# Kernel tuning notes

Measured on AMD Instinct MI355X. Metric: run time of the kernel, lower is better.

The kernel has to match this reference:

```python
import jax, jax.numpy as jnp
import numpy as np

N_NODES = 100000
D_FEAT = 128
N_EDGES = 1600000


def setup_inputs() -> dict:
    key = jax.random.key(0)
    k1, k2, k3 = jax.random.split(key, 3)
    x = jax.random.normal(k1, (N_NODES, D_FEAT), dtype=jnp.float32)
    edge_weight = jax.random.uniform(k2, (N_EDGES,), dtype=jnp.float32)
    edge_index = jax.random.randint(k3, (2, N_EDGES), 0, N_NODES, dtype=jnp.int64)
    return {"x": x, "edge_weight": edge_weight, "edge_index": edge_index, "n_nodes": N_NODES}


def reference(x, edge_weight, edge_index, n_nodes):
    # h_v = sum_{(u->v) in E} w_uv * h_u  (gather -> scale -> scatter_add)
    src = edge_index[0]
    dst = edge_index[1]
    msg = x[src] * edge_weight[:, None]          # (E, d)
    out = jax.ops.segment_sum(msg, dst, num_segments=n_nodes)  # (N, d)
    return out
```

## Files before the change

### kernel.cpp

```cpp
#include <hip/hip_runtime.h>
#include <hip/hip_bf16.h>


constexpr int D_FEAT = 128;
constexpr int NPB = 128;
constexpr int SBLK = 256;
constexpr int LOG_SBLK = 8;
constexpr int STILE = 2048;
constexpr int CAP = 3072;

typedef float v4f __attribute__((ext_vector_type(4)));

__global__ __launch_bounds__(256) void scatter_atomic_kernel(
    const float* __restrict__ x, const float* __restrict__ w,
    const int* __restrict__ src_idx, const int* __restrict__ dst_idx,
    float* __restrict__ out, int n_edges) {
  long long tid = (long long)blockIdx.x * blockDim.x + threadIdx.x;
  int lane = (int)(tid & 31);
  long long e = tid >> 5;
  if (e >= n_edges) return;
  int s = src_idx[e];
  int d = dst_idx[e];
  float wt = w[e];
  float4 v = ((const float4*)(x + (size_t)s * D_FEAT))[lane];
  float* o = out + (size_t)d * D_FEAT + (size_t)lane * 4;
  atomicAdd(o + 0, v.x * wt);
  atomicAdd(o + 1, v.y * wt);
  atomicAdd(o + 2, v.z * wt);
  atomicAdd(o + 3, v.w * wt);
}

__device__ __forceinline__ int block_excl_scan(int v, int* sh, int* total) {
  const int lane = threadIdx.x & 63;
  const int wid = threadIdx.x >> 6;
  const int nw = blockDim.x >> 6;
  int inc = v;
  #pragma unroll
  for (int o = 1; o < 64; o <<= 1) {
    int t = __shfl_up(inc, o, 64);
    if (lane >= o) inc += t;
  }
  if (lane == 63) sh[wid] = inc;
  __syncthreads();
  if (threadIdx.x == 0) {
    int a = 0;
    for (int k = 0; k < nw; ++k) { int t = sh[k]; sh[k] = a; a += t; }
    sh[nw] = a;
  }
  __syncthreads();
  int r = sh[wid] + inc - v;
  if (total) *total = sh[nw];
  __syncthreads();
  return r;
}

__global__ __launch_bounds__(512) void hist_kernel(
    const int* __restrict__ dst, int* __restrict__ hist, int n_edges,
    int nbk, int tile) {
  __shared__ int h[1024];
  const int tid = threadIdx.x;
  const int b = blockIdx.x;
  for (int i = tid; i < nbk; i += 512) h[i] = 0;
  __syncthreads();
  int base = b * tile;
  int lim = min(base + tile, n_edges);
  for (int i = base + tid; i < lim; i += 512)
    atomicAdd(&h[((unsigned)dst[i]) >> 7], 1);
  __syncthreads();
  for (int k = tid; k < nbk; k += 512) hist[b * nbk + k] = h[k];
}

__global__ __launch_bounds__(256) void scan_kernel(
    const int* __restrict__ hist, int* __restrict__ off_flat,
    unsigned long long* __restrict__ tstate, int nbk, int n_edges) {
  __shared__ int sh[9];
  __shared__ int s_prefix;
  const int tid = threadIdx.x;
  const int blk = blockIdx.x;
  const int n_scan = nbk * SBLK;
  const int base = blk * STILE + tid * 8;

  int c[8];
  #pragma unroll
  for (int k = 0; k < 8; ++k) {
    int i = base + k;
    c[k] = (i < n_scan) ? hist[(i & (SBLK - 1)) * nbk + (i >> LOG_SBLK)] : 0;
  }
  int p[8];
  int tsum = 0;
  #pragma unroll
  for (int k = 0; k < 8; ++k) { p[k] = tsum; tsum += c[k]; }

  int total;
  int tex = block_excl_scan(tsum, sh, &total);

  if (tid == 0) {
    int excl = 0;
    if (blk == 0) {
      __hip_atomic_store(&tstate[0], (2ULL << 32) | (unsigned)total,
                         __ATOMIC_RELEASE, __HIP_MEMORY_SCOPE_AGENT);
    } else {
      __hip_atomic_store(&tstate[blk], (1ULL << 32) | (unsigned)total,
                         __ATOMIC_RELEASE, __HIP_MEMORY_SCOPE_AGENT);
      int pidx = blk - 1;
      int run = 0;
      while (true) {
        unsigned long long v = __hip_atomic_load(
            &tstate[pidx], __ATOMIC_ACQUIRE, __HIP_MEMORY_SCOPE_AGENT);
        unsigned st = (unsigned)(v >> 32);
        if (st != 1u && st != 2u) { __builtin_amdgcn_s_sleep(1); continue; }
        run += (int)(unsigned)v;
        if (st == 2u) break;
        --pidx;
      }
      excl = run;
      __hip_atomic_store(&tstate[blk],
                         (2ULL << 32) | (unsigned)(excl + total),
                         __ATOMIC_RELEASE, __HIP_MEMORY_SCOPE_AGENT);
    }
    s_prefix = excl;
  }
  __syncthreads();

  int my = s_prefix + tex;
  if (base + 8 <= n_scan) {
    ((int4*)(off_flat + base))[0] =
        make_int4(my + p[0], my + p[1], my + p[2], my + p[3]);
    ((int4*)(off_flat + base))[1] =
        make_int4(my + p[4], my + p[5], my + p[6], my + p[7]);
  } else {
    #pragma unroll
    for (int k = 0; k < 8; ++k)
      if (base + k < n_scan) off_flat[base + k] = my + p[k];
  }
  if (blk == 0 && tid == 0) off_flat[n_scan] = n_edges;
}

__global__ __launch_bounds__(512) void scatter_kernel(
    const int* __restrict__ src, const int* __restrict__ dst,
    const float* __restrict__ w, const int* __restrict__ off_flat,
    uint2* __restrict__ csr, int n_edges, int nbk, int tile) {
  __shared__ int cur[1024];
  const int tid = threadIdx.x;
  const int b = blockIdx.x;
  for (int k = tid; k < nbk; k += 512) cur[k] = off_flat[k * SBLK + b];
  __syncthreads();
  int base = b * tile;
  int lim = min(base + tile, n_edges);
  for (int i = base + tid; i < lim; i += 512) {
    unsigned d = (unsigned)dst[i];
    unsigned k = d >> 7;
    unsigned dl = d & 127u;
    int pos = atomicAdd(&cur[k], 1);
    csr[pos] = make_uint2((unsigned)src[i] | (dl << 20), __float_as_uint(w[i]));
  }
}

__global__ __launch_bounds__(512) void gather_kernel(
    const float* __restrict__ x, const int* __restrict__ off_flat,
    const uint2* __restrict__ csr, float* __restrict__ out, int n_nodes) {
  __shared__ uint2 eds[CAP];
  __shared__ unsigned short perm[CAP];
  __shared__ int loff[NPB + 1];
  __shared__ int lcur[NPB];
  __shared__ int sh[9];

  const int b = blockIdx.x;
  const int tid = threadIdx.x;
  const int beg = off_flat[b * SBLK];
  const int end = off_flat[(b + 1) * SBLK];
  const int cnt = end - beg;
  const int nbase = b * NPB;

  const int wv = tid >> 6;
  const int lane = tid & 63;
  const int f = lane & 31;
  const int half = lane >> 5;
  const float4* X = (const float4*)x;

  if (cnt <= CAP) {
    if (tid < NPB) lcur[tid] = 0;
    __syncthreads();
    for (int i = tid; i < cnt; i += 512) {
      uint2 e = csr[beg + i];
      eds[i] = e;
      atomicAdd(&lcur[e.x >> 20], 1);
    }
    __syncthreads();
    {
      int v = (tid < NPB) ? lcur[tid] : 0;
      int ex = block_excl_scan(v, sh, nullptr);
      __syncthreads();
      if (tid < NPB) { loff[tid] = ex; lcur[tid] = 0; }
      if (tid == 0) loff[NPB] = cnt;
    }
    __syncthreads();
    for (int i = tid; i < cnt; i += 512) {
      int dl = eds[i].x >> 20;
      int pos = loff[dl] + atomicAdd(&lcur[dl], 1);
      perm[pos] = (unsigned short)i;
    }
    __syncthreads();

    for (int n = wv; n < NPB; n += 8) {
      int node = nbase + n;
      if (node >= n_nodes) break;
      int jb = loff[n];
      int je = loff[n + 1];
      float4 a0 = make_float4(0.f, 0.f, 0.f, 0.f);
      float4 a1 = make_float4(0.f, 0.f, 0.f, 0.f);
      float4 a2 = make_float4(0.f, 0.f, 0.f, 0.f);
      float4 a3 = make_float4(0.f, 0.f, 0.f, 0.f);
      int j = jb + half;
      for (; j + 6 < je; j += 8) {
        uint2 e0 = eds[perm[j]];
        uint2 e1 = eds[perm[j + 2]];
        uint2 e2 = eds[perm[j + 4]];
        uint2 e3 = eds[perm[j + 6]];
        float4 v0 = X[(size_t)(e0.x & 0xFFFFFu) * 32 + f];
        float4 v1 = X[(size_t)(e1.x & 0xFFFFFu) * 32 + f];
        float4 v2 = X[(size_t)(e2.x & 0xFFFFFu) * 32 + f];
        float4 v3 = X[(size_t)(e3.x & 0xFFFFFu) * 32 + f];
        float w0 = __uint_as_float(e0.y);
        float w1 = __uint_as_float(e1.y);
        float w2 = __uint_as_float(e2.y);
        float w3 = __uint_as_float(e3.y);
        a0.x += w0 * v0.x; a0.y += w0 * v0.y; a0.z += w0 * v0.z; a0.w += w0 * v0.w;
        a1.x += w1 * v1.x; a1.y += w1 * v1.y; a1.z += w1 * v1.z; a1.w += w1 * v1.w;
        a2.x += w2 * v2.x; a2.y += w2 * v2.y; a2.z += w2 * v2.z; a2.w += w2 * v2.w;
        a3.x += w3 * v3.x; a3.y += w3 * v3.y; a3.z += w3 * v3.z; a3.w += w3 * v3.w;
      }
      for (; j < je; j += 2) {
        uint2 e0 = eds[perm[j]];
        float4 v0 = X[(size_t)(e0.x & 0xFFFFFu) * 32 + f];
        float w0 = __uint_as_float(e0.y);
        a0.x += w0 * v0.x; a0.y += w0 * v0.y; a0.z += w0 * v0.z; a0.w += w0 * v0.w;
      }
      a0.x += a1.x + a2.x + a3.x;
      a0.y += a1.y + a2.y + a3.y;
      a0.z += a1.z + a2.z + a3.z;
      a0.w += a1.w + a2.w + a3.w;
      a0.x += __shfl_xor(a0.x, 32, 64);
      a0.y += __shfl_xor(a0.y, 32, 64);
      a0.z += __shfl_xor(a0.z, 32, 64);
      a0.w += __shfl_xor(a0.w, 32, 64);
      if (half == 0) {
        v4f val = {a0.x, a0.y, a0.z, a0.w};
        __builtin_nontemporal_store(val, (v4f*)out + (size_t)node * 32 + f);
      }
    }
  } else {
    for (int n = wv; n < NPB; n += 8) {
      int node = nbase + n;
      if (node >= n_nodes) break;
      float4 a0 = make_float4(0.f, 0.f, 0.f, 0.f);
      for (int j = half; j < cnt; j += 2) {
        uint2 e = csr[beg + j];
        if ((int)(e.x >> 20) == n) {
          float4 v = X[(size_t)(e.x & 0xFFFFFu) * 32 + f];
          float wt = __uint_as_float(e.y);
          a0.x += wt * v.x; a0.y += wt * v.y; a0.z += wt * v.z; a0.w += wt * v.w;
        }
      }
      a0.x += __shfl_xor(a0.x, 32, 64);
      a0.y += __shfl_xor(a0.y, 32, 64);
      a0.z += __shfl_xor(a0.z, 32, 64);
      a0.w += __shfl_xor(a0.w, 32, 64);
      if (half == 0) {
        v4f val = {a0.x, a0.y, a0.z, a0.w};
        __builtin_nontemporal_store(val, (v4f*)out + (size_t)node * 32 + f);
      }
    }
  }
}

extern "C" void kernel_launch(void* const* d_in, const int* in_sizes, int n_in,
                              void* d_out, int out_size, void* d_ws, size_t ws_size,
                              hipStream_t stream) {
  const float* x  = (const float*)d_in[0];
  const float* w  = (const float*)d_in[1];
  const int* eidx = (const int*)d_in[2];

  int n_edges = in_sizes[1];
  int n_nodes = out_size / D_FEAT;
  const int* src = eidx;
  const int* dst = eidx + n_edges;
  float* out = (float*)d_out;

  const int nbk = (n_nodes + NPB - 1) / NPB;
  const int tile = (n_edges + SBLK - 1) / SBLK;
  const int n_scan = nbk * SBLK;
  const int ntiles = (n_scan + STILE - 1) / STILE;

  const size_t n_hist = (size_t)SBLK * nbk;
  const size_t n_off = (size_t)n_scan + 4;
  size_t need = (n_hist + n_off) * 4 + 128 * 8 + (size_t)n_edges * 8;
  if (ws_size < need || nbk > 1024 || ntiles > 128 || n_nodes >= (1 << 20)) {
    hipMemsetAsync(d_out, 0, (size_t)out_size * sizeof(float), stream);
    long long total_threads = (long long)n_edges * 32;
    long long grid = (total_threads + 255) / 256;
    scatter_atomic_kernel<<<(dim3)(unsigned)grid, 256, 0, stream>>>(
        x, w, src, dst, out, n_edges);
    return;
  }

  int* hist = (int*)d_ws;
  int* off_flat = hist + n_hist;
  unsigned long long* tstate = (unsigned long long*)(off_flat + n_off);
  uint2* csr = (uint2*)(tstate + 128);

  hist_kernel<<<SBLK, 512, 0, stream>>>(dst, hist, n_edges, nbk, tile);
  scan_kernel<<<ntiles, 256, 0, stream>>>(hist, off_flat, tstate, nbk,
                                          n_edges);
  scatter_kernel<<<SBLK, 512, 0, stream>>>(src, dst, w, off_flat, csr,
                                           n_edges, nbk, tile);
  gather_kernel<<<nbk, 512, 0, stream>>>(x, off_flat, csr, out, n_nodes);
}
```

Before: 269.0 us.

## Split gather blocks by feature half and parallelize scan lookback across a wavefront

```diff
diff --git a/kernel.cpp b/kernel.cpp
--- a/kernel.cpp
+++ b/kernel.cpp
@@ -94,31 +94,49 @@
   int total;
   int tex = block_excl_scan(tsum, sh, &total);
 
-  if (tid == 0) {
-    int excl = 0;
-    if (blk == 0) {
+  if (blk == 0) {
+    if (tid == 0) {
       __hip_atomic_store(&tstate[0], (2ULL << 32) | (unsigned)total,
                          __ATOMIC_RELEASE, __HIP_MEMORY_SCOPE_AGENT);
-    } else {
+      s_prefix = 0;
+    }
+  } else {
+    if (tid == 0)
       __hip_atomic_store(&tstate[blk], (1ULL << 32) | (unsigned)total,
                          __ATOMIC_RELEASE, __HIP_MEMORY_SCOPE_AGENT);
-      int pidx = blk - 1;
+    if (tid < 64) {
+      int pidx = blk - 1 - tid;
       int run = 0;
       while (true) {
-        unsigned long long v = __hip_atomic_load(
-            &tstate[pidx], __ATOMIC_ACQUIRE, __HIP_MEMORY_SCOPE_AGENT);
-        unsigned st = (unsigned)(v >> 32);
-        if (st != 1u && st != 2u) { __builtin_amdgcn_s_sleep(1); continue; }
-        run += (int)(unsigned)v;
-        if (st == 2u) break;
-        --pidx;
-      }
-      excl = run;
-      __hip_atomic_store(&tstate[blk],
-                         (2ULL << 32) | (unsigned)(excl + total),
-                         __ATOMIC_RELEASE, __HIP_MEMORY_SCOPE_AGENT);
-    }
-    s_prefix = excl;
+        unsigned long long v;
+        unsigned st;
+        if (pidx >= 0) {
+          do {
+            v = __hip_atomic_load(&tstate[pidx], __ATOMIC_ACQUIRE,
+                                  __HIP_MEMORY_SCOPE_AGENT);
+            st = (unsigned)(v >> 32);
+            if (st != 1u && st != 2u) __builtin_amdgcn_s_sleep(1);
+          } while (st != 1u && st != 2u);
+        } else {
+          v = (2ULL << 32);
+          st = 2u;
+        }
+        unsigned long long pmask = __ballot(st == 2u);
+        int lfirst = (int)__ffsll((long long)pmask) - 1;
+        int contrib = (lfirst < 0 || tid <= lfirst) ? (int)(unsigned)v : 0;
+        #pragma unroll
+        for (int o = 32; o; o >>= 1) contrib += __shfl_xor(contrib, o, 64);
+        run += contrib;
+        if (lfirst >= 0) break;
+        pidx -= 64;
+      }
+      if (tid == 0) {
+        __hip_atomic_store(&tstate[blk],
+                           (2ULL << 32) | (unsigned)(run + total),
+                           __ATOMIC_RELEASE, __HIP_MEMORY_SCOPE_AGENT);
+        s_prefix = run;
+      }
+    }
   }
   __syncthreads();
 
@@ -156,7 +174,7 @@
   }
 }
 
-__global__ __launch_bounds__(512) void gather_kernel(
+__global__ __launch_bounds__(256) void gather_kernel(
     const float* __restrict__ x, const int* __restrict__ off_flat,
     const uint2* __restrict__ csr, float* __restrict__ out, int n_nodes) {
   __shared__ uint2 eds[CAP];
@@ -165,7 +183,8 @@
   __shared__ int lcur[NPB];
   __shared__ int sh[9];
 
-  const int b = blockIdx.x;
+  const int b = blockIdx.x >> 1;
+  const int fh = blockIdx.x & 1;
   const int tid = threadIdx.x;
   const int beg = off_flat[b * SBLK];
   const int end = off_flat[(b + 1) * SBLK];
@@ -174,14 +193,14 @@
 
   const int wv = tid >> 6;
   const int lane = tid & 63;
-  const int f = lane & 31;
-  const int half = lane >> 5;
+  const int q = lane >> 4;
+  const int f = (lane & 15) + fh * 16;
   const float4* X = (const float4*)x;
 
   if (cnt <= CAP) {
     if (tid < NPB) lcur[tid] = 0;
     __syncthreads();
-    for (int i = tid; i < cnt; i += 512) {
+    for (int i = tid; i < cnt; i += 256) {
       uint2 e = csr[beg + i];
       eds[i] = e;
       atomicAdd(&lcur[e.x >> 20], 1);
@@ -195,14 +214,14 @@
       if (tid == 0) loff[NPB] = cnt;
     }
     __syncthreads();
-    for (int i = tid; i < cnt; i += 512) {
+    for (int i = tid; i < cnt; i += 256) {
       int dl = eds[i].x >> 20;
       int pos = loff[dl] + atomicAdd(&lcur[dl], 1);
       perm[pos] = (unsigned short)i;
     }
     __syncthreads();
 
-    for (int n = wv; n < NPB; n += 8) {
+    for (int n = wv; n < NPB; n += 4) {
       int node = nbase + n;
       if (node >= n_nodes) break;
       int jb = loff[n];
@@ -211,12 +230,12 @@
       float4 a1 = make_float4(0.f, 0.f, 0.f, 0.f);
       float4 a2 = make_float4(0.f, 0.f, 0.f, 0.f);
       float4 a3 = make_float4(0.f, 0.f, 0.f, 0.f);
-      int j = jb + half;
-      for (; j + 6 < je; j += 8) {
+      int j = jb + q;
+      for (; j + 12 < je; j += 16) {
         uint2 e0 = eds[perm[j]];
-        uint2 e1 = eds[perm[j + 2]];
-        uint2 e2 = eds[perm[j + 4]];
-        uint2 e3 = eds[perm[j + 6]];
+        uint2 e1 = eds[perm[j + 4]];
+        uint2 e2 = eds[perm[j + 8]];
+        uint2 e3 = eds[perm[j + 12]];
         float4 v0 = X[(size_t)(e0.x & 0xFFFFFu) * 32 + f];
         float4 v1 = X[(size_t)(e1.x & 0xFFFFFu) * 32 + f];
         float4 v2 = X[(size_t)(e2.x & 0xFFFFFu) * 32 + f];
@@ -230,7 +249,7 @@
         a2.x += w2 * v2.x; a2.y += w2 * v2.y; a2.z += w2 * v2.z; a2.w += w2 * v2.w;
         a3.x += w3 * v3.x; a3.y += w3 * v3.y; a3.z += w3 * v3.z; a3.w += w3 * v3.w;
       }
-      for (; j < je; j += 2) {
+      for (; j < je; j += 4) {
         uint2 e0 = eds[perm[j]];
         float4 v0 = X[(size_t)(e0.x & 0xFFFFFu) * 32 + f];
         float w0 = __uint_as_float(e0.y);
@@ -240,21 +259,25 @@
       a0.y += a1.y + a2.y + a3.y;
       a0.z += a1.z + a2.z + a3.z;
       a0.w += a1.w + a2.w + a3.w;
+      a0.x += __shfl_xor(a0.x, 16, 64);
+      a0.y += __shfl_xor(a0.y, 16, 64);
+      a0.z += __shfl_xor(a0.z, 16, 64);
+      a0.w += __shfl_xor(a0.w, 16, 64);
       a0.x += __shfl_xor(a0.x, 32, 64);
       a0.y += __shfl_xor(a0.y, 32, 64);
       a0.z += __shfl_xor(a0.z, 32, 64);
       a0.w += __shfl_xor(a0.w, 32, 64);
-      if (half == 0) {
+      if (q == 0) {
         v4f val = {a0.x, a0.y, a0.z, a0.w};
         __builtin_nontemporal_store(val, (v4f*)out + (size_t)node * 32 + f);
       }
     }
   } else {
-    for (int n = wv; n < NPB; n += 8) {
+    for (int n = wv; n < NPB; n += 4) {
       int node = nbase + n;
       if (node >= n_nodes) break;
       float4 a0 = make_float4(0.f, 0.f, 0.f, 0.f);
-      for (int j = half; j < cnt; j += 2) {
+      for (int j = q; j < cnt; j += 4) {
         uint2 e = csr[beg + j];
         if ((int)(e.x >> 20) == n) {
           float4 v = X[(size_t)(e.x & 0xFFFFFu) * 32 + f];
@@ -262,11 +285,15 @@
           a0.x += wt * v.x; a0.y += wt * v.y; a0.z += wt * v.z; a0.w += wt * v.w;
         }
       }
+      a0.x += __shfl_xor(a0.x, 16, 64);
+      a0.y += __shfl_xor(a0.y, 16, 64);
+      a0.z += __shfl_xor(a0.z, 16, 64);
+      a0.w += __shfl_xor(a0.w, 16, 64);
       a0.x += __shfl_xor(a0.x, 32, 64);
       a0.y += __shfl_xor(a0.y, 32, 64);
       a0.z += __shfl_xor(a0.z, 32, 64);
       a0.w += __shfl_xor(a0.w, 32, 64);
-      if (half == 0) {
+      if (q == 0) {
         v4f val = {a0.x, a0.y, a0.z, a0.w};
         __builtin_nontemporal_store(val, (v4f*)out + (size_t)node * 32 + f);
       }
@@ -314,5 +341,5 @@
                                           n_edges);
   scatter_kernel<<<SBLK, 512, 0, stream>>>(src, dst, w, off_flat, csr,
                                            n_edges, nbk, tile);
-  gather_kernel<<<nbk, 512, 0, stream>>>(x, off_flat, csr, out, n_nodes);
-}
+  gather_kernel<<<nbk * 2, 256, 0, stream>>>(x, off_flat, csr, out, n_nodes);
+}
```

Result: no change. 267.4 us (-0.6%).

## Replace per-block histogram scan with global bucket counts and LDS-staged coalesced scatter

Applied to the files above, without the earlier changes.

```diff
diff --git a/kernel.cpp b/kernel.cpp
--- a/kernel.cpp
+++ b/kernel.cpp
@@ -1,12 +1,11 @@
 #include <hip/hip_runtime.h>
-#include <hip/hip_bf16.h>
 
 
 constexpr int D_FEAT = 128;
 constexpr int NPB = 128;
-constexpr int SBLK = 256;
-constexpr int LOG_SBLK = 8;
-constexpr int STILE = 2048;
+constexpr int NBK_MAX = 1024;
+constexpr int HBLK = 256;
+constexpr int CTILE = 3136;
 constexpr int CAP = 3072;
 
 typedef float v4f __attribute__((ext_vector_type(4)));
@@ -55,109 +54,109 @@
 }
 
 __global__ __launch_bounds__(512) void hist_kernel(
-    const int* __restrict__ dst, int* __restrict__ hist, int n_edges,
-    int nbk, int tile) {
-  __shared__ int h[1024];
+    const int* __restrict__ dst, int* __restrict__ gtot,
+    int* __restrict__ gcur, int* __restrict__ gbase, int* __restrict__ done,
+    int n_edges, int nbk, int tile) {
+  __shared__ int h[NBK_MAX];
+  __shared__ int sh[9];
+  __shared__ int slast;
   const int tid = threadIdx.x;
   const int b = blockIdx.x;
-  for (int i = tid; i < nbk; i += 512) h[i] = 0;
+  for (int k = tid; k < nbk; k += 512) h[k] = 0;
   __syncthreads();
   int base = b * tile;
   int lim = min(base + tile, n_edges);
   for (int i = base + tid; i < lim; i += 512)
     atomicAdd(&h[((unsigned)dst[i]) >> 7], 1);
   __syncthreads();
-  for (int k = tid; k < nbk; k += 512) hist[b * nbk + k] = h[k];
-}
-
-__global__ __launch_bounds__(256) void scan_kernel(
-    const int* __restrict__ hist, int* __restrict__ off_flat,
-    unsigned long long* __restrict__ tstate, int nbk, int n_edges) {
-  __shared__ int sh[9];
-  __shared__ int s_prefix;
-  const int tid = threadIdx.x;
-  const int blk = blockIdx.x;
-  const int n_scan = nbk * SBLK;
-  const int base = blk * STILE + tid * 8;
-
-  int c[8];
-  #pragma unroll
-  for (int k = 0; k < 8; ++k) {
-    int i = base + k;
-    c[k] = (i < n_scan) ? hist[(i & (SBLK - 1)) * nbk + (i >> LOG_SBLK)] : 0;
-  }
-  int p[8];
-  int tsum = 0;
-  #pragma unroll
-  for (int k = 0; k < 8; ++k) { p[k] = tsum; tsum += c[k]; }
-
-  int total;
-  int tex = block_excl_scan(tsum, sh, &total);
-
-  if (tid == 0) {
-    int excl = 0;
-    if (blk == 0) {
-      __hip_atomic_store(&tstate[0], (2ULL << 32) | (unsigned)total,
-                         __ATOMIC_RELEASE, __HIP_MEMORY_SCOPE_AGENT);
-    } else {
-      __hip_atomic_store(&tstate[blk], (1ULL << 32) | (unsigned)total,
-                         __ATOMIC_RELEASE, __HIP_MEMORY_SCOPE_AGENT);
-      int pidx = blk - 1;
-      int run = 0;
-      while (true) {
-        unsigned long long v = __hip_atomic_load(
-            &tstate[pidx], __ATOMIC_ACQUIRE, __HIP_MEMORY_SCOPE_AGENT);
-        unsigned st = (unsigned)(v >> 32);
-        if (st != 1u && st != 2u) { __builtin_amdgcn_s_sleep(1); continue; }
-        run += (int)(unsigned)v;
-        if (st == 2u) break;
-        --pidx;
-      }
-      excl = run;
-      __hip_atomic_store(&tstate[blk],
-                         (2ULL << 32) | (unsigned)(excl + total),
-                         __ATOMIC_RELEASE, __HIP_MEMORY_SCOPE_AGENT);
-    }
-    s_prefix = excl;
-  }
-  __syncthreads();
-
-  int my = s_prefix + tex;
-  if (base + 8 <= n_scan) {
-    ((int4*)(off_flat + base))[0] =
-        make_int4(my + p[0], my + p[1], my + p[2], my + p[3]);
-    ((int4*)(off_flat + base))[1] =
-        make_int4(my + p[4], my + p[5], my + p[6], my + p[7]);
-  } else {
-    #pragma unroll
-    for (int k = 0; k < 8; ++k)
-      if (base + k < n_scan) off_flat[base + k] = my + p[k];
-  }
-  if (blk == 0 && tid == 0) off_flat[n_scan] = n_edges;
+  for (int k = tid; k < nbk; k += 512)
+    if (h[k]) atomicAdd(&gtot[k], h[k]);
+  __threadfence();
+  __syncthreads();
+  if (tid == 0)
+    slast = (__hip_atomic_fetch_add(done, 1, __ATOMIC_ACQ_REL,
+                                    __HIP_MEMORY_SCOPE_AGENT) ==
+             (int)gridDim.x - 1);
+  __syncthreads();
+  if (slast) {
+    int carry = 0;
+    for (int kb = 0; kb < nbk; kb += 512) {
+      int k = kb + tid;
+      int v = (k < nbk)
+                  ? __hip_atomic_load(&gtot[k], __ATOMIC_RELAXED,
+                                      __HIP_MEMORY_SCOPE_AGENT)
+                  : 0;
+      int tot;
+      int ex = block_excl_scan(v, sh, &tot);
+      if (k < nbk) { gbase[k] = carry + ex; gcur[k] = carry + ex; }
+      carry += tot;
+    }
+    if (tid == 0) gbase[nbk] = carry;
+  }
 }
 
 __global__ __launch_bounds__(512) void scatter_kernel(
     const int* __restrict__ src, const int* __restrict__ dst,
-    const float* __restrict__ w, const int* __restrict__ off_flat,
+    const float* __restrict__ w, int* __restrict__ gcur,
     uint2* __restrict__ csr, int n_edges, int nbk, int tile) {
-  __shared__ int cur[1024];
+  __shared__ uint2 ed[CTILE];
+  __shared__ unsigned short bkt[CTILE];
+  __shared__ unsigned int prm[CTILE];
+  __shared__ int h[NBK_MAX];
+  __shared__ int lb[NBK_MAX];
+  __shared__ int cur[NBK_MAX];
+  __shared__ int gb[NBK_MAX];
+  __shared__ int sh[9];
+
   const int tid = threadIdx.x;
   const int b = blockIdx.x;
-  for (int k = tid; k < nbk; k += 512) cur[k] = off_flat[k * SBLK + b];
-  __syncthreads();
   int base = b * tile;
   int lim = min(base + tile, n_edges);
+  int cnt = max(lim - base, 0);
+
+  for (int k = tid; k < nbk; k += 512) { h[k] = 0; cur[k] = 0; }
+  __syncthreads();
   for (int i = base + tid; i < lim; i += 512) {
+    int j = i - base;
     unsigned d = (unsigned)dst[i];
     unsigned k = d >> 7;
-    unsigned dl = d & 127u;
-    int pos = atomicAdd(&cur[k], 1);
-    csr[pos] = make_uint2((unsigned)src[i] | (dl << 20), __float_as_uint(w[i]));
-  }
-}
-
-__global__ __launch_bounds__(512) void gather_kernel(
-    const float* __restrict__ x, const int* __restrict__ off_flat,
+    ed[j] = make_uint2((unsigned)src[i] | ((d & 127u) << 20),
+                       __float_as_uint(w[i]));
+    bkt[j] = (unsigned short)k;
+    atomicAdd(&h[k], 1);
+  }
+  __syncthreads();
+  {
+    int carry = 0;
+    for (int kb = 0; kb < nbk; kb += 512) {
+      int k = kb + tid;
+      int v = (k < nbk) ? h[k] : 0;
+      int tot;
+      int ex = block_excl_scan(v, sh, &tot);
+      if (k < nbk) {
+        lb[k] = carry + ex;
+        if (v) gb[k] = atomicAdd(&gcur[k], v);
+      }
+      carry += tot;
+    }
+  }
+  __syncthreads();
+  for (int j = tid; j < cnt; j += 512) {
+    int k = bkt[j];
+    int oc = atomicAdd(&cur[k], 1);
+    prm[lb[k] + oc] = (unsigned)j | ((unsigned)k << 12);
+  }
+  __syncthreads();
+  for (int p = tid; p < cnt; p += 512) {
+    unsigned v = prm[p];
+    int j = (int)(v & 0xFFFu);
+    int k = (int)(v >> 12);
+    csr[gb[k] + (p - lb[k])] = ed[j];
+  }
+}
+
+__global__ __launch_bounds__(256) void gather_kernel(
+    const float* __restrict__ x, const int* __restrict__ gbase,
     const uint2* __restrict__ csr, float* __restrict__ out, int n_nodes) {
   __shared__ uint2 eds[CAP];
   __shared__ unsigned short perm[CAP];
@@ -167,8 +166,8 @@
 
   const int b = blockIdx.x;
   const int tid = threadIdx.x;
-  const int beg = off_flat[b * SBLK];
-  const int end = off_flat[(b + 1) * SBLK];
+  const int beg = gbase[b];
+  const int end = gbase[b + 1];
   const int cnt = end - beg;
   const int nbase = b * NPB;
 
@@ -181,7 +180,7 @@
   if (cnt <= CAP) {
     if (tid < NPB) lcur[tid] = 0;
     __syncthreads();
-    for (int i = tid; i < cnt; i += 512) {
+    for (int i = tid; i < cnt; i += 256) {
       uint2 e = csr[beg + i];
       eds[i] = e;
       atomicAdd(&lcur[e.x >> 20], 1);
@@ -195,14 +194,14 @@
       if (tid == 0) loff[NPB] = cnt;
     }
     __syncthreads();
-    for (int i = tid; i < cnt; i += 512) {
+    for (int i = tid; i < cnt; i += 256) {
       int dl = eds[i].x >> 20;
       int pos = loff[dl] + atomicAdd(&lcur[dl], 1);
       perm[pos] = (unsigned short)i;
     }
     __syncthreads();
 
-    for (int n = wv; n < NPB; n += 8) {
+    for (int n = wv; n < NPB; n += 4) {
       int node = nbase + n;
       if (node >= n_nodes) break;
       int jb = loff[n];
@@ -250,7 +249,7 @@
       }
     }
   } else {
-    for (int n = wv; n < NPB; n += 8) {
+    for (int n = wv; n < NPB; n += 4) {
       int node = nbase + n;
       if (node >= n_nodes) break;
       float4 a0 = make_float4(0.f, 0.f, 0.f, 0.f);
@@ -288,14 +287,18 @@
   float* out = (float*)d_out;
 
   const int nbk = (n_nodes + NPB - 1) / NPB;
-  const int tile = (n_edges + SBLK - 1) / SBLK;
-  const int n_scan = nbk * SBLK;
-  const int ntiles = (n_scan + STILE - 1) / STILE;
-
-  const size_t n_hist = (size_t)SBLK * nbk;
-  const size_t n_off = (size_t)n_scan + 4;
-  size_t need = (n_hist + n_off) * 4 + 128 * 8 + (size_t)n_edges * 8;
-  if (ws_size < need || nbk > 1024 || ntiles > 128 || n_nodes >= (1 << 20)) {
+  const int htile = (n_edges + HBLK - 1) / HBLK;
+  const int cblk = (n_edges + CTILE - 11 - 1) / (CTILE - 11);
+  const int ctile = cblk > 0 ? (n_edges + cblk - 1) / cblk : 0;
+
+  const size_t ctrl_ints = 1024 + 1024 + 4 + 1028;
+  size_t need = ctrl_ints * 4 + (size_t)n_edges * 8;
+  if (n_edges <= 0) {
+    hipMemsetAsync(d_out, 0, (size_t)out_size * sizeof(float), stream);
+    return;
+  }
+  if (ws_size < need || nbk > NBK_MAX || n_nodes >= (1 << 20) ||
+      ctile > CTILE) {
     hipMemsetAsync(d_out, 0, (size_t)out_size * sizeof(float), stream);
     long long total_threads = (long long)n_edges * 32;
     long long grid = (total_threads + 255) / 256;
@@ -304,15 +307,17 @@
     return;
   }
 
-  int* hist = (int*)d_ws;
-  int* off_flat = hist + n_hist;
-  unsigned long long* tstate = (unsigned long long*)(off_flat + n_off);
-  uint2* csr = (uint2*)(tstate + 128);
-
-  hist_kernel<<<SBLK, 512, 0, stream>>>(dst, hist, n_edges, nbk, tile);
-  scan_kernel<<<ntiles, 256, 0, stream>>>(hist, off_flat, tstate, nbk,
-                                          n_edges);
-  scatter_kernel<<<SBLK, 512, 0, stream>>>(src, dst, w, off_flat, csr,
-                                           n_edges, nbk, tile);
-  gather_kernel<<<nbk, 512, 0, stream>>>(x, off_flat, csr, out, n_nodes);
-}
+  int* gtot = (int*)d_ws;
+  int* gcur = gtot + 1024;
+  int* done = gcur + 1024;
+  int* gbase = done + 4;
+  uint2* csr = (uint2*)(gbase + 1028);
+
+  hipMemsetAsync(gtot, 0, (1024 + 1024 + 4) * sizeof(int), stream);
+
+  hist_kernel<<<HBLK, 512, 0, stream>>>(dst, gtot, gcur, gbase, done,
+                                        n_edges, nbk, htile);
+  scatter_kernel<<<cblk, 512, 0, stream>>>(src, dst, w, gcur, csr,
+                                           n_edges, nbk, ctile);
+  gather_kernel<<<nbk, 256, 0, stream>>>(x, gbase, csr, out, n_nodes);
+}
```

Measured after the change: 279.6 us. 3.9% more time.
